# Kernel optimization log

Hardware: AMD Instinct MI355X
Metric: run time of the kernel (lower is better)

The kernel has to match this reference:

```python
import jax, jax.numpy as jnp
import numpy as np

NEG_SLOPE = 0.2  # PyG GATConv default negative_slope


def _gat_conv(x, src, dst, W, a_src, a_dst, bias, heads, concat):
    """PyG-style GATConv (eval mode, self-loops already appended to src/dst).
    x: [N, Fin], W: [Fin, heads*C], a_src/a_dst: [heads, C], bias matches output.
    """
    N = x.shape[0]
    C = W.shape[1] // heads
    xw = (x @ W).reshape(N, heads, C)                      # [N, H, C]
    alpha_s = jnp.sum(xw * a_src, axis=-1)                 # [N, H]
    alpha_d = jnp.sum(xw * a_dst, axis=-1)                 # [N, H]
    e = jax.nn.leaky_relu(alpha_s[src] + alpha_d[dst], NEG_SLOPE)  # [E, H]
    # softmax over incoming edges of each destination node (numerically stable)
    m = jax.ops.segment_max(e, dst, num_segments=N)        # [N, H]
    e = jnp.exp(e - m[dst])
    denom = jax.ops.segment_sum(e, dst, num_segments=N)    # [N, H]
    alpha = e / denom[dst]                                 # [E, H]
    out = jax.ops.segment_sum(alpha[:, :, None] * xw[src], dst, num_segments=N)  # [N, H, C]
    if concat:
        out = out.reshape(N, heads * C)
    else:
        out = out.mean(axis=1)
    return out + bias


def setup_inputs() -> dict:
    key = jax.random.key(0)
    ks = jax.random.split(key, 10)
    N, E, FIN, FOUT, H1, C1 = 100000, 1600000, 128, 16, 4, 8
    x = jax.random.normal(ks[0], (N, FIN), jnp.float32)
    edge_index = jax.random.randint(ks[1], (2, E), 0, N, dtype=jnp.int32)
    W1 = jax.random.normal(ks[2], (FIN, H1 * C1), jnp.float32) / np.sqrt(FIN)
    a1_src = jax.random.normal(ks[3], (H1, C1), jnp.float32) / np.sqrt(C1)
    a1_dst = jax.random.normal(ks[4], (H1, C1), jnp.float32) / np.sqrt(C1)
    b1 = jnp.zeros((H1 * C1,), jnp.float32)
    W2 = jax.random.normal(ks[5], (H1 * C1, FOUT), jnp.float32) / np.sqrt(H1 * C1)
    a2_src = jax.random.normal(ks[6], (1, FOUT), jnp.float32) / np.sqrt(FOUT)
    a2_dst = jax.random.normal(ks[7], (1, FOUT), jnp.float32) / np.sqrt(FOUT)
    b2 = jnp.zeros((FOUT,), jnp.float32)
    return {"x": x, "edge_index": edge_index, "W1": W1, "a1_src": a1_src,
            "a1_dst": a1_dst, "b1": b1, "W2": W2, "a2_src": a2_src,
            "a2_dst": a2_dst, "b2": b2}


def reference(x, edge_index, W1, a1_src, a1_dst, b1, W2, a2_src, a2_dst, b2):
    N = x.shape[0]
    # PyG GATConv add_self_loops=True default
    loop = jnp.arange(N, dtype=edge_index.dtype)
    src = jnp.concatenate([edge_index[0], loop])
    dst = jnp.concatenate([edge_index[1], loop])
    # eval mode: F.dropout is identity
    h = _gat_conv(x, src, dst, W1, a1_src, a1_dst, b1, heads=4, concat=True)
    h = jax.nn.elu(h)
    h = _gat_conv(h, src, dst, W2, a2_src, a2_dst, b2, heads=1, concat=True)
    return jax.nn.log_softmax(h, axis=1)
```

## Files before the change

### kernel.cpp

```cpp
#include <hip/hip_runtime.h>
#include <math.h>

#define NN 100000
#define NE 1600000
#define ET (NE + NN)
#define FIN 128
#define H1 4
#define C1 8
#define F1 32
#define FOUT 16
#define NSLOPE 0.2f

#define PARTW 256
#define PSHIFT 8
#define NPART ((NN + PARTW - 1) / PARTW)
#define CHUNK 8192
#define NBLK ((ET + CHUNK - 1) / CHUNK)
#define CPAD 16
#define SMASK 0x1FFFF

typedef _Float16 half8 __attribute__((ext_vector_type(8)));
typedef float f32x4 __attribute__((ext_vector_type(4)));


__device__ inline int wave_incl_scan(int v) {
#pragma unroll
    for (int off = 1; off < 64; off <<= 1) {
        int u = __shfl_up(v, off);
        if ((threadIdx.x & 63) >= off) v += u;
    }
    return v;
}

__device__ inline int block_excl_scan(int v, int* wsum, int nw) {
    int t = threadIdx.x, wid = t >> 6, lane = t & 63;
    int incl = wave_incl_scan(v);
    if (lane == 63) wsum[wid] = incl;
    __syncthreads();
    if (wid == 0) {
        int wv = (lane < nw) ? wsum[lane] : 0;
        wv = wave_incl_scan(wv);
        if (lane < nw) wsum[lane] = wv;
    }
    __syncthreads();
    return incl - v + (wid ? wsum[wid - 1] : 0);
}


__global__ __launch_bounds__(1024) void k_hist(const int* __restrict__ dstA, int* __restrict__ ptotal) {
    __shared__ int h[NPART];
    int t = threadIdx.x;
    for (int i = t; i < NPART; i += 1024) h[i] = 0;
    __syncthreads();
    int base = blockIdx.x * CHUNK;
#pragma unroll
    for (int k = 0; k < CHUNK / 1024; k++) {
        int e = base + k * 1024 + t;
        if (e < ET) {
            int d = (e < NE) ? dstA[e] : (e - NE);
            atomicAdd(&h[d >> PSHIFT], 1);
        }
    }
    __syncthreads();
    for (int i = t; i < NPART; i += 1024)
        if (h[i]) atomicAdd(&ptotal[i * CPAD], h[i]);
}

__global__ __launch_bounds__(512) void k_pbase(const int* __restrict__ ptotal, int* __restrict__ pbase,
                                               int* __restrict__ gcur, int* __restrict__ rowstart) {
    __shared__ int wsum[8];
    int t = threadIdx.x;
    int v = (t < NPART) ? ptotal[t * CPAD] : 0;
    int excl = block_excl_scan(v, wsum, 8);
    if (t < NPART) { pbase[t] = excl; gcur[t * CPAD] = excl; }
    if (t == 0) { pbase[NPART] = ET; rowstart[NN] = ET; }
}

__global__ __launch_bounds__(1024) void k_part(const int* __restrict__ srcA, const int* __restrict__ dstA,
                                               int* __restrict__ gcur, int* __restrict__ pairs) {
    __shared__ int h[NPART];
    __shared__ int cur[NPART];
    int t = threadIdx.x;
    for (int i = t; i < NPART; i += 1024) h[i] = 0;
    __syncthreads();
    int base = blockIdx.x * CHUNK;
#pragma unroll
    for (int k = 0; k < CHUNK / 1024; k++) {
        int e = base + k * 1024 + t;
        if (e < ET) {
            int d = (e < NE) ? dstA[e] : (e - NE);
            atomicAdd(&h[d >> PSHIFT], 1);
        }
    }
    __syncthreads();
    for (int i = t; i < NPART; i += 1024) {
        int c = h[i];
        cur[i] = c ? atomicAdd(&gcur[i * CPAD], c) : 0;
    }
    __syncthreads();
#pragma unroll
    for (int k = 0; k < CHUNK / 1024; k++) {
        int e = base + k * 1024 + t;
        if (e < ET) {
            int s, d;
            if (e < NE) { s = srcA[e]; d = dstA[e]; }
            else        { s = e - NE;  d = s; }
            int pos = atomicAdd(&cur[d >> PSHIFT], 1);
            pairs[pos] = ((d & (PARTW - 1)) << 17) | s;
        }
    }
}

__global__ __launch_bounds__(1024) void k_sort(const int* __restrict__ pbase, const int* __restrict__ pairs,
                                               int* __restrict__ rowstart, int* __restrict__ epack) {
    __shared__ int hist[PARTW];
    __shared__ int sa[PARTW], sb[PARTW];
    int p = blockIdx.x;
    int t = threadIdx.x;
    int n0 = p << PSHIFT;
    int nn = min(PARTW, NN - n0);
    int base = pbase[p];
    int cnt = pbase[p + 1] - base;
    if (t < PARTW) hist[t] = 0;
    __syncthreads();
    for (int i = t; i < cnt; i += 1024)
        atomicAdd(&hist[pairs[base + i] >> 17], 1);
    __syncthreads();
    if (t < PARTW) sa[t] = hist[t];
    __syncthreads();
    int* pin = sa; int* pout = sb;
    for (int off = 1; off < PARTW; off <<= 1) {
        if (t < PARTW) pout[t] = pin[t] + ((t >= off) ? pin[t - off] : 0);
        __syncthreads();
        int* tmp = pin; pin = pout; pout = tmp;
    }
    int excl = 0;
    if (t < PARTW) {
        excl = pin[t] - hist[t];
        if (t < nn) rowstart[n0 + t] = base + excl;
    }
    __syncthreads();
    if (t < PARTW) hist[t] = excl;
    __syncthreads();
    for (int i = t; i < cnt; i += 1024) {
        int v = pairs[base + i];
        int pos = base + atomicAdd(&hist[v >> 17], 1);
        epack[pos] = v;
    }
}


__global__ __launch_bounds__(256) void k_gemm1(const float* __restrict__ x, const float* __restrict__ W1,
        const float* __restrict__ a1s, const float* __restrict__ a1d,
        _Float16* __restrict__ xw1h, float* __restrict__ as1, float* __restrict__ ad1) {
    __shared__ _Float16 w1t[F1 * FIN];
    __shared__ float xs[256 * F1];
    int t = threadIdx.x;
    {
        int i0 = t * 16;
#pragma unroll
        for (int i = 0; i < 16; i++) {
            int idx = i0 + i;
            int k = idx >> 5, n = idx & 31;
            w1t[n * FIN + k] = (_Float16)W1[idx];
        }
    }
    __syncthreads();
    int w = t >> 6, l = t & 63;
    int q = l >> 4, r16 = l & 15;
    int nblk = blockIdx.x * 256;
    int n0 = nblk + w * 64;
    half8 bf[4][2];
#pragma unroll
    for (int kc = 0; kc < 4; kc++)
#pragma unroll
        for (int nt = 0; nt < 2; nt++)
            bf[kc][nt] = *(const half8*)&w1t[(nt * 16 + r16) * FIN + kc * 32 + q * 8];
#pragma unroll
    for (int mt = 0; mt < 4; mt++) {
        int row = n0 + mt * 16 + r16;
        int rowc = min(row, NN - 1);
        const float4* xp = (const float4*)(x + (size_t)rowc * FIN + q * 8);
        half8 af[4];
#pragma unroll
        for (int kc = 0; kc < 4; kc++) {
            float4 u = xp[kc * 8];
            float4 v = xp[kc * 8 + 1];
            half8 a;
            a[0] = (_Float16)u.x; a[1] = (_Float16)u.y; a[2] = (_Float16)u.z; a[3] = (_Float16)u.w;
            a[4] = (_Float16)v.x; a[5] = (_Float16)v.y; a[6] = (_Float16)v.z; a[7] = (_Float16)v.w;
            af[kc] = a;
        }
        f32x4 acc0 = {0.f, 0.f, 0.f, 0.f};
        f32x4 acc1 = {0.f, 0.f, 0.f, 0.f};
#pragma unroll
        for (int kc = 0; kc < 4; kc++) {
            acc0 = __builtin_amdgcn_mfma_f32_16x16x32_f16(af[kc], bf[kc][0], acc0, 0, 0, 0);
            acc1 = __builtin_amdgcn_mfma_f32_16x16x32_f16(af[kc], bf[kc][1], acc1, 0, 0, 0);
        }
#pragma unroll
        for (int r = 0; r < 4; r++) {
            xs[(w * 64 + mt * 16 + q * 4 + r) * F1 + r16] = acc0[r];
            xs[(w * 64 + mt * 16 + q * 4 + r) * F1 + 16 + r16] = acc1[r];
        }
    }
    int node = nblk + w * 64 + l;
    if (node < NN) {
        const float4* xr = (const float4*)&xs[(w * 64 + l) * F1];
        float rowv[F1];
#pragma unroll
        for (int j = 0; j < 8; j++) {
            float4 v = xr[j];
            rowv[j * 4] = v.x; rowv[j * 4 + 1] = v.y; rowv[j * 4 + 2] = v.z; rowv[j * 4 + 3] = v.w;
        }
        half8* o8 = (half8*)(xw1h + (size_t)node * F1);
#pragma unroll
        for (int c8 = 0; c8 < F1 / 8; c8++) {
            half8 o;
#pragma unroll
            for (int k = 0; k < 8; k++) o[k] = (_Float16)rowv[c8 * 8 + k];
            o8[c8] = o;
        }
        float ss[H1], dd[H1];
#pragma unroll
        for (int h = 0; h < H1; h++) {
            ss[h] = 0.f; dd[h] = 0.f;
#pragma unroll
            for (int c = 0; c < C1; c++) {
                ss[h] = fmaf(rowv[h * C1 + c], a1s[h * C1 + c], ss[h]);
                dd[h] = fmaf(rowv[h * C1 + c], a1d[h * C1 + c], dd[h]);
            }
        }
        ((float4*)as1)[node] = make_float4(ss[0], ss[1], ss[2], ss[3]);
        ((float4*)ad1)[node] = make_float4(dd[0], dd[1], dd[2], dd[3]);
    }
}


__global__ __launch_bounds__(256) void k_gather1(const int* __restrict__ rowstart, const int* __restrict__ epack,
        const float* __restrict__ as1, const float* __restrict__ ad1,
        const _Float16* __restrict__ xw1h, const float* __restrict__ b1,
        _Float16* __restrict__ h1h) {
    int n = blockIdx.x * 4 + (threadIdx.x >> 6);
    if (n >= NN) return;
    int l = threadIdx.x & 63;
    int c = l & 31;
    int h = c >> 3;
    int half = l >> 5;
    float adh = ad1[n * H1 + h];
    int beg = rowstart[n], end = rowstart[n + 1];
    float accn = 0.f, accd = 0.f;
    int i = beg + half;
    for (; i + 6 < end; i += 8) {
        int s0 = epack[i] & SMASK, s1 = epack[i + 2] & SMASK;
        int s2 = epack[i + 4] & SMASK, s3 = epack[i + 6] & SMASK;
        float e0 = as1[s0 * H1 + h] + adh;
        float e1 = as1[s1 * H1 + h] + adh;
        float e2 = as1[s2 * H1 + h] + adh;
        float e3 = as1[s3 * H1 + h] + adh;
        float x0 = (float)xw1h[s0 * F1 + c];
        float x1 = (float)xw1h[s1 * F1 + c];
        float x2 = (float)xw1h[s2 * F1 + c];
        float x3 = (float)xw1h[s3 * F1 + c];
        e0 = (e0 > 0.f) ? e0 : NSLOPE * e0;
        e1 = (e1 > 0.f) ? e1 : NSLOPE * e1;
        e2 = (e2 > 0.f) ? e2 : NSLOPE * e2;
        e3 = (e3 > 0.f) ? e3 : NSLOPE * e3;
        float ee0 = __expf(e0), ee1 = __expf(e1), ee2 = __expf(e2), ee3 = __expf(e3);
        accd += (ee0 + ee1) + (ee2 + ee3);
        accn = fmaf(ee0, x0, fmaf(ee1, x1, fmaf(ee2, x2, fmaf(ee3, x3, accn))));
    }
    for (; i < end; i += 2) {
        int s0 = epack[i] & SMASK;
        float e0 = as1[s0 * H1 + h] + adh;
        float x0 = (float)xw1h[s0 * F1 + c];
        e0 = (e0 > 0.f) ? e0 : NSLOPE * e0;
        float ee0 = __expf(e0);
        accd += ee0;
        accn = fmaf(ee0, x0, accn);
    }
    accn += __shfl_xor(accn, 32);
    accd += __shfl_xor(accd, 32);
    float y = accn / accd + b1[c];
    y = (y > 0.f) ? y : expm1f(y);
    if (l < 32) h1h[(size_t)n * F1 + c] = (_Float16)y;
}


__global__ __launch_bounds__(256) void k_node2(const _Float16* __restrict__ h1h, const float* __restrict__ W2,
        const float* __restrict__ a2s, const float* __restrict__ a2d,
        _Float16* __restrict__ xw2h, float* __restrict__ as2, float* __restrict__ ad2) {
    int n = blockIdx.x * 256 + threadIdx.x;
    if (n >= NN) return;
    float acc[FOUT];
#pragma unroll
    for (int j = 0; j < FOUT; j++) acc[j] = 0.f;
    const half8* h8 = (const half8*)(h1h + (size_t)n * F1);
#pragma unroll
    for (int i8 = 0; i8 < F1 / 8; i8++) {
        half8 hv = h8[i8];
#pragma unroll
        for (int kk = 0; kk < 8; kk++) {
            float hk = (float)hv[kk];
            int i = i8 * 8 + kk;
#pragma unroll
            for (int j = 0; j < FOUT; j++)
                acc[j] = fmaf(hk, W2[i * FOUT + j], acc[j]);
        }
    }
    float ss = 0.f, dd = 0.f;
#pragma unroll
    for (int j = 0; j < FOUT; j++) {
        ss = fmaf(acc[j], a2s[j], ss);
        dd = fmaf(acc[j], a2d[j], dd);
    }
    half8* o8 = (half8*)(xw2h + (size_t)n * FOUT);
#pragma unroll
    for (int j8 = 0; j8 < FOUT / 8; j8++) {
        half8 o;
#pragma unroll
        for (int k = 0; k < 8; k++) o[k] = (_Float16)acc[j8 * 8 + k];
        o8[j8] = o;
    }
    as2[n] = ss;
    ad2[n] = dd;
}


__global__ __launch_bounds__(256) void k_gather2(const int* __restrict__ rowstart, const int* __restrict__ epack,
        const float* __restrict__ as2, const float* __restrict__ ad2,
        const _Float16* __restrict__ xw2h, const float* __restrict__ b2,
        float* __restrict__ out) {
    int n = blockIdx.x * 4 + (threadIdx.x >> 6);
    if (n >= NN) return;
    int l = threadIdx.x & 63;
    int c = l & 15;
    int q = l >> 4;
    float adn = ad2[n];
    int beg = rowstart[n], end = rowstart[n + 1];
    float accn = 0.f, accd = 0.f;
    int i = beg + q;
    for (; i + 12 < end; i += 16) {
        int s0 = epack[i] & SMASK, s1 = epack[i + 4] & SMASK;
        int s2 = epack[i + 8] & SMASK, s3 = epack[i + 12] & SMASK;
        float e0 = as2[s0] + adn;
        float e1 = as2[s1] + adn;
        float e2 = as2[s2] + adn;
        float e3 = as2[s3] + adn;
        float x0 = (float)xw2h[s0 * FOUT + c];
        float x1 = (float)xw2h[s1 * FOUT + c];
        float x2 = (float)xw2h[s2 * FOUT + c];
        float x3 = (float)xw2h[s3 * FOUT + c];
        e0 = (e0 > 0.f) ? e0 : NSLOPE * e0;
        e1 = (e1 > 0.f) ? e1 : NSLOPE * e1;
        e2 = (e2 > 0.f) ? e2 : NSLOPE * e2;
        e3 = (e3 > 0.f) ? e3 : NSLOPE * e3;
        float ee0 = __expf(e0), ee1 = __expf(e1), ee2 = __expf(e2), ee3 = __expf(e3);
        accd += (ee0 + ee1) + (ee2 + ee3);
        accn = fmaf(ee0, x0, fmaf(ee1, x1, fmaf(ee2, x2, fmaf(ee3, x3, accn))));
    }
    for (; i < end; i += 4) {
        int s0 = epack[i] & SMASK;
        float e0 = as2[s0] + adn;
        float x0 = (float)xw2h[s0 * FOUT + c];
        e0 = (e0 > 0.f) ? e0 : NSLOPE * e0;
        float ee0 = __expf(e0);
        accd += ee0;
        accn = fmaf(ee0, x0, accn);
    }
    accn += __shfl_xor(accn, 16);
    accn += __shfl_xor(accn, 32);
    accd += __shfl_xor(accd, 16);
    accd += __shfl_xor(accd, 32);
    float y = accn / accd + b2[c];
    float m = y;
#pragma unroll
    for (int off = 8; off > 0; off >>= 1) m = fmaxf(m, __shfl_xor(m, off));
    float ex = __expf(y - m);
    float sum = ex;
#pragma unroll
    for (int off = 8; off > 0; off >>= 1) sum += __shfl_xor(sum, off);
    if (l < 16) out[(size_t)n * FOUT + c] = y - m - logf(sum);
}


extern "C" void kernel_launch(void* const* d_in, const int* in_sizes, int n_in,
                              void* d_out, int out_size, void* d_ws, size_t ws_size,
                              hipStream_t stream) {
    const float* x   = (const float*)d_in[0];
    const int*   ei  = (const int*)d_in[1];
    const float* W1  = (const float*)d_in[2];
    const float* a1s = (const float*)d_in[3];
    const float* a1d = (const float*)d_in[4];
    const float* b1  = (const float*)d_in[5];
    const float* W2  = (const float*)d_in[6];
    const float* a2s = (const float*)d_in[7];
    const float* a2d = (const float*)d_in[8];
    const float* b2  = (const float*)d_in[9];
    float* out = (float*)d_out;

    const int* srcA = ei;
    const int* dstA = ei + NE;

    char* w = (char*)d_ws;
    size_t off = 0;
    auto carve = [&](size_t bytes) -> void* {
        void* p = w + off;
        off = (off + bytes + 255) & ~(size_t)255;
        return p;
    };
    _Float16* xw1h = (_Float16*)carve((size_t)NN * F1 * 2);
    float* as1     = (float*)carve((size_t)NN * H1 * 4);
    float* ad1     = (float*)carve((size_t)NN * H1 * 4);
    size_t h1_off  = off;
    _Float16* h1h  = (_Float16*)carve((size_t)NN * F1 * 2);
    _Float16* xw2h = (_Float16*)carve((size_t)NN * FOUT * 2);
    float* as2     = (float*)carve((size_t)NN * 4);
    float* ad2     = (float*)carve((size_t)NN * 4);
    int* pairs     = (int*)(w + h1_off);
    int* rowstart  = (int*)carve((size_t)(NN + 1) * 4);
    int* epack     = (int*)carve((size_t)ET * 4);
    int* ptotal    = (int*)carve((size_t)NPART * CPAD * 4);
    int* gcur      = (int*)carve((size_t)NPART * CPAD * 4);
    int* pbase     = (int*)carve((size_t)(NPART + 1) * 4);
    (void)ws_size; (void)in_sizes; (void)n_in; (void)out_size;

    hipMemsetAsync(ptotal, 0, (size_t)NPART * CPAD * 4, stream);

    k_hist  <<<NBLK, 1024, 0, stream>>>(dstA, ptotal);
    k_pbase <<<1, 512, 0, stream>>>(ptotal, pbase, gcur, rowstart);
    k_part  <<<NBLK, 1024, 0, stream>>>(srcA, dstA, gcur, pairs);
    k_sort  <<<NPART, 1024, 0, stream>>>(pbase, pairs, rowstart, epack);

    k_gemm1 <<<(NN + 255) / 256, 256, 0, stream>>>(x, W1, a1s, a1d, xw1h, as1, ad1);
    k_gather1<<<(NN + 3) / 4, 256, 0, stream>>>(rowstart, epack, as1, ad1, xw1h, b1, h1h);
    k_node2 <<<(NN + 255) / 256, 256, 0, stream>>>(h1h, W2, a2s, a2d, xw2h, as2, ad2);
    k_gather2<<<(NN + 3) / 4, 256, 0, stream>>>(rowstart, epack, as2, ad2, xw2h, b2, out);
}
```

Baseline: 257.6 us.

## Fuse CSR build and first GEMM into one cooperative kernel with grid syncs

Replaces the memset, histogram, partition-base scan, partition scatter, per-partition sort and first-layer GEMM kernels with a single cooperative kernel of 512 blocks of 256 threads. The stages are separated by grid-wide syncs, and the partition scan now runs as a single wave. The aim is to remove several kernel launches and their inter-kernel gaps. In exchange, each stage now uses smaller blocks (the sort uses 256 threads per partition instead of 1024), every stage pays a grid-sync cost, and the whole grid must stay co-resident.

After: 501.1 us. +94.5%, slower.

```diff
diff --git a/kernel.cpp b/kernel.cpp
--- a/kernel.cpp
+++ b/kernel.cpp
@@ -1,5 +1,8 @@
 #include <hip/hip_runtime.h>
+#include <hip/hip_cooperative_groups.h>
 #include <math.h>
+
+namespace cg = cooperative_groups;
 
 #define NN 100000
 #define NE 1600000
@@ -14,14 +17,14 @@
 #define PARTW 256
 #define PSHIFT 8
 #define NPART ((NN + PARTW - 1) / PARTW)
-#define CHUNK 8192
-#define NBLK ((ET + CHUNK - 1) / CHUNK)
 #define CPAD 16
 #define SMASK 0x1FFFF
 
+#define K1B 512
+#define EB ((ET + K1B - 1) / K1B)
+
 typedef _Float16 half8 __attribute__((ext_vector_type(8)));
 typedef float f32x4 __attribute__((ext_vector_type(4)));
-
 
 __device__ inline int wave_incl_scan(int v) {
 #pragma unroll
@@ -32,207 +35,186 @@
     return v;
 }
 
-__device__ inline int block_excl_scan(int v, int* wsum, int nw) {
-    int t = threadIdx.x, wid = t >> 6, lane = t & 63;
-    int incl = wave_incl_scan(v);
-    if (lane == 63) wsum[wid] = incl;
-    __syncthreads();
-    if (wid == 0) {
-        int wv = (lane < nw) ? wsum[lane] : 0;
-        wv = wave_incl_scan(wv);
-        if (lane < nw) wsum[lane] = wv;
-    }
-    __syncthreads();
-    return incl - v + (wid ? wsum[wid - 1] : 0);
-}
-
-
-__global__ __launch_bounds__(1024) void k_hist(const int* __restrict__ dstA, int* __restrict__ ptotal) {
-    __shared__ int h[NPART];
-    int t = threadIdx.x;
-    for (int i = t; i < NPART; i += 1024) h[i] = 0;
-    __syncthreads();
-    int base = blockIdx.x * CHUNK;
-#pragma unroll
-    for (int k = 0; k < CHUNK / 1024; k++) {
-        int e = base + k * 1024 + t;
-        if (e < ET) {
-            int d = (e < NE) ? dstA[e] : (e - NE);
-            atomicAdd(&h[d >> PSHIFT], 1);
-        }
-    }
-    __syncthreads();
-    for (int i = t; i < NPART; i += 1024)
-        if (h[i]) atomicAdd(&ptotal[i * CPAD], h[i]);
-}
-
-__global__ __launch_bounds__(512) void k_pbase(const int* __restrict__ ptotal, int* __restrict__ pbase,
-                                               int* __restrict__ gcur, int* __restrict__ rowstart) {
-    __shared__ int wsum[8];
-    int t = threadIdx.x;
-    int v = (t < NPART) ? ptotal[t * CPAD] : 0;
-    int excl = block_excl_scan(v, wsum, 8);
-    if (t < NPART) { pbase[t] = excl; gcur[t * CPAD] = excl; }
-    if (t == 0) { pbase[NPART] = ET; rowstart[NN] = ET; }
-}
-
-__global__ __launch_bounds__(1024) void k_part(const int* __restrict__ srcA, const int* __restrict__ dstA,
-                                               int* __restrict__ gcur, int* __restrict__ pairs) {
+
+__global__ __launch_bounds__(256) void k_build(const int* __restrict__ srcA, const int* __restrict__ dstA,
+        const float* __restrict__ x, const float* __restrict__ W1,
+        const float* __restrict__ a1s, const float* __restrict__ a1d,
+        int* __restrict__ ptotal, int* __restrict__ gcur, int* __restrict__ pbase,
+        int* __restrict__ rowstart, int* __restrict__ pairs, int* __restrict__ epack,
+        _Float16* __restrict__ xw1h, float* __restrict__ as1, float* __restrict__ ad1) {
+    cg::grid_group grid = cg::this_grid();
     __shared__ int h[NPART];
     __shared__ int cur[NPART];
-    int t = threadIdx.x;
-    for (int i = t; i < NPART; i += 1024) h[i] = 0;
-    __syncthreads();
-    int base = blockIdx.x * CHUNK;
-#pragma unroll
-    for (int k = 0; k < CHUNK / 1024; k++) {
-        int e = base + k * 1024 + t;
-        if (e < ET) {
-            int d = (e < NE) ? dstA[e] : (e - NE);
-            atomicAdd(&h[d >> PSHIFT], 1);
-        }
-    }
-    __syncthreads();
-    for (int i = t; i < NPART; i += 1024) {
-        int c = h[i];
-        cur[i] = c ? atomicAdd(&gcur[i * CPAD], c) : 0;
-    }
-    __syncthreads();
-#pragma unroll
-    for (int k = 0; k < CHUNK / 1024; k++) {
-        int e = base + k * 1024 + t;
-        if (e < ET) {
-            int s, d;
-            if (e < NE) { s = srcA[e]; d = dstA[e]; }
-            else        { s = e - NE;  d = s; }
-            int pos = atomicAdd(&cur[d >> PSHIFT], 1);
-            pairs[pos] = ((d & (PARTW - 1)) << 17) | s;
-        }
-    }
-}
-
-__global__ __launch_bounds__(1024) void k_sort(const int* __restrict__ pbase, const int* __restrict__ pairs,
-                                               int* __restrict__ rowstart, int* __restrict__ epack) {
-    __shared__ int hist[PARTW];
-    __shared__ int sa[PARTW], sb[PARTW];
-    int p = blockIdx.x;
-    int t = threadIdx.x;
-    int n0 = p << PSHIFT;
-    int nn = min(PARTW, NN - n0);
-    int base = pbase[p];
-    int cnt = pbase[p + 1] - base;
-    if (t < PARTW) hist[t] = 0;
-    __syncthreads();
-    for (int i = t; i < cnt; i += 1024)
-        atomicAdd(&hist[pairs[base + i] >> 17], 1);
-    __syncthreads();
-    if (t < PARTW) sa[t] = hist[t];
-    __syncthreads();
-    int* pin = sa; int* pout = sb;
-    for (int off = 1; off < PARTW; off <<= 1) {
-        if (t < PARTW) pout[t] = pin[t] + ((t >= off) ? pin[t - off] : 0);
-        __syncthreads();
-        int* tmp = pin; pin = pout; pout = tmp;
-    }
-    int excl = 0;
-    if (t < PARTW) {
-        excl = pin[t] - hist[t];
-        if (t < nn) rowstart[n0 + t] = base + excl;
-    }
-    __syncthreads();
-    if (t < PARTW) hist[t] = excl;
-    __syncthreads();
-    for (int i = t; i < cnt; i += 1024) {
-        int v = pairs[base + i];
-        int pos = base + atomicAdd(&hist[v >> 17], 1);
-        epack[pos] = v;
-    }
-}
-
-
-__global__ __launch_bounds__(256) void k_gemm1(const float* __restrict__ x, const float* __restrict__ W1,
-        const float* __restrict__ a1s, const float* __restrict__ a1d,
-        _Float16* __restrict__ xw1h, float* __restrict__ as1, float* __restrict__ ad1) {
+    __shared__ int sc[PARTW];
     __shared__ _Float16 w1t[F1 * FIN];
     __shared__ float xs[256 * F1];
     int t = threadIdx.x;
+    int b = blockIdx.x;
+    int e0 = b * EB, e1 = min(e0 + EB, ET);
+
     {
-        int i0 = t * 16;
-#pragma unroll
-        for (int i = 0; i < 16; i++) {
-            int idx = i0 + i;
-            int k = idx >> 5, n = idx & 31;
-            w1t[n * FIN + k] = (_Float16)W1[idx];
-        }
-    }
+        int idx = b * 256 + t;
+        if (idx < NPART) ptotal[idx * CPAD] = 0;
+    }
+    grid.sync();
+
+    for (int i = t; i < NPART; i += 256) h[i] = 0;
     __syncthreads();
-    int w = t >> 6, l = t & 63;
-    int q = l >> 4, r16 = l & 15;
-    int nblk = blockIdx.x * 256;
-    int n0 = nblk + w * 64;
-    half8 bf[4][2];
-#pragma unroll
-    for (int kc = 0; kc < 4; kc++)
-#pragma unroll
-        for (int nt = 0; nt < 2; nt++)
-            bf[kc][nt] = *(const half8*)&w1t[(nt * 16 + r16) * FIN + kc * 32 + q * 8];
-#pragma unroll
-    for (int mt = 0; mt < 4; mt++) {
-        int row = n0 + mt * 16 + r16;
-        int rowc = min(row, NN - 1);
-        const float4* xp = (const float4*)(x + (size_t)rowc * FIN + q * 8);
-        half8 af[4];
-#pragma unroll
-        for (int kc = 0; kc < 4; kc++) {
-            float4 u = xp[kc * 8];
-            float4 v = xp[kc * 8 + 1];
-            half8 a;
-            a[0] = (_Float16)u.x; a[1] = (_Float16)u.y; a[2] = (_Float16)u.z; a[3] = (_Float16)u.w;
-            a[4] = (_Float16)v.x; a[5] = (_Float16)v.y; a[6] = (_Float16)v.z; a[7] = (_Float16)v.w;
-            af[kc] = a;
-        }
-        f32x4 acc0 = {0.f, 0.f, 0.f, 0.f};
-        f32x4 acc1 = {0.f, 0.f, 0.f, 0.f};
-#pragma unroll
-        for (int kc = 0; kc < 4; kc++) {
-            acc0 = __builtin_amdgcn_mfma_f32_16x16x32_f16(af[kc], bf[kc][0], acc0, 0, 0, 0);
-            acc1 = __builtin_amdgcn_mfma_f32_16x16x32_f16(af[kc], bf[kc][1], acc1, 0, 0, 0);
-        }
-#pragma unroll
-        for (int r = 0; r < 4; r++) {
-            xs[(w * 64 + mt * 16 + q * 4 + r) * F1 + r16] = acc0[r];
-            xs[(w * 64 + mt * 16 + q * 4 + r) * F1 + 16 + r16] = acc1[r];
-        }
-    }
-    int node = nblk + w * 64 + l;
-    if (node < NN) {
-        const float4* xr = (const float4*)&xs[(w * 64 + l) * F1];
-        float rowv[F1];
-#pragma unroll
-        for (int j = 0; j < 8; j++) {
-            float4 v = xr[j];
-            rowv[j * 4] = v.x; rowv[j * 4 + 1] = v.y; rowv[j * 4 + 2] = v.z; rowv[j * 4 + 3] = v.w;
-        }
-        half8* o8 = (half8*)(xw1h + (size_t)node * F1);
-#pragma unroll
-        for (int c8 = 0; c8 < F1 / 8; c8++) {
-            half8 o;
-#pragma unroll
-            for (int k = 0; k < 8; k++) o[k] = (_Float16)rowv[c8 * 8 + k];
-            o8[c8] = o;
-        }
-        float ss[H1], dd[H1];
-#pragma unroll
-        for (int h = 0; h < H1; h++) {
-            ss[h] = 0.f; dd[h] = 0.f;
-#pragma unroll
-            for (int c = 0; c < C1; c++) {
-                ss[h] = fmaf(rowv[h * C1 + c], a1s[h * C1 + c], ss[h]);
-                dd[h] = fmaf(rowv[h * C1 + c], a1d[h * C1 + c], dd[h]);
-            }
-        }
-        ((float4*)as1)[node] = make_float4(ss[0], ss[1], ss[2], ss[3]);
-        ((float4*)ad1)[node] = make_float4(dd[0], dd[1], dd[2], dd[3]);
+    for (int e = e0 + t; e < e1; e += 256) {
+        int d = (e < NE) ? dstA[e] : (e - NE);
+        atomicAdd(&h[d >> PSHIFT], 1);
+    }
+    __syncthreads();
+    for (int i = t; i < NPART; i += 256)
+        if (h[i]) atomicAdd(&ptotal[i * CPAD], h[i]);
+    grid.sync();
+
+    if (b == 0 && t < 64) {
+        int base = t * 7;
+        int loc[7]; int s = 0;
+#pragma unroll
+        for (int i = 0; i < 7; i++) {
+            int idx = base + i;
+            int v = (idx < NPART) ? ptotal[idx * CPAD] : 0;
+            loc[i] = s; s += v;
+        }
+        int wex = wave_incl_scan(s) - s;
+#pragma unroll
+        for (int i = 0; i < 7; i++) {
+            int idx = base + i;
+            if (idx < NPART) { pbase[idx] = wex + loc[i]; gcur[idx * CPAD] = wex + loc[i]; }
+        }
+        if (t == 0) { pbase[NPART] = ET; rowstart[NN] = ET; }
+    }
+    grid.sync();
+
+    for (int i = t; i < NPART; i += 256) {
+        int c = h[i];
+        cur[i] = c ? atomicAdd(&gcur[i * CPAD], c) : 0;
+    }
+    __syncthreads();
+    for (int e = e0 + t; e < e1; e += 256) {
+        int s, d;
+        if (e < NE) { s = srcA[e]; d = dstA[e]; }
+        else        { s = e - NE;  d = s; }
+        int pos = atomicAdd(&cur[d >> PSHIFT], 1);
+        pairs[pos] = ((d & (PARTW - 1)) << 17) | s;
+    }
+    grid.sync();
+
+    if (b < NPART) {
+        int n0 = b << PSHIFT;
+        int nn = min(PARTW, NN - n0);
+        int base = pbase[b];
+        int cnt = pbase[b + 1] - base;
+        if (t < PARTW) h[t] = 0;
+        __syncthreads();
+        for (int i = t; i < cnt; i += 256)
+            atomicAdd(&h[pairs[base + i] >> 17], 1);
+        __syncthreads();
+        if (t < PARTW) cur[t] = h[t];
+        __syncthreads();
+        int* pin = cur; int* pout = sc;
+        for (int off = 1; off < PARTW; off <<= 1) {
+            if (t < PARTW) pout[t] = pin[t] + ((t >= off) ? pin[t - off] : 0);
+            __syncthreads();
+            int* tmp = pin; pin = pout; pout = tmp;
+        }
+        int excl = 0;
+        if (t < PARTW) {
+            excl = pin[t] - h[t];
+            if (t < nn) rowstart[n0 + t] = base + excl;
+        }
+        __syncthreads();
+        if (t < PARTW) h[t] = excl;
+        __syncthreads();
+        for (int i = t; i < cnt; i += 256) {
+            int v = pairs[base + i];
+            int pos = base + atomicAdd(&h[v >> 17], 1);
+            epack[pos] = v;
+        }
+        __syncthreads();
+    }
+
+    if (b * 256 < NN) {
+        {
+            int i0 = t * 16;
+#pragma unroll
+            for (int i = 0; i < 16; i++) {
+                int idx = i0 + i;
+                int k = idx >> 5, n = idx & 31;
+                w1t[n * FIN + k] = (_Float16)W1[idx];
+            }
+        }
+        __syncthreads();
+        int w = t >> 6, l = t & 63;
+        int q = l >> 4, r16 = l & 15;
+        int nblk = b * 256;
+        int n0 = nblk + w * 64;
+        half8 bf[4][2];
+#pragma unroll
+        for (int kc = 0; kc < 4; kc++)
+#pragma unroll
+            for (int nt = 0; nt < 2; nt++)
+                bf[kc][nt] = *(const half8*)&w1t[(nt * 16 + r16) * FIN + kc * 32 + q * 8];
+#pragma unroll
+        for (int mt = 0; mt < 4; mt++) {
+            int row = n0 + mt * 16 + r16;
+            int rowc = min(row, NN - 1);
+            const float4* xp = (const float4*)(x + (size_t)rowc * FIN + q * 8);
+            half8 af[4];
+#pragma unroll
+            for (int kc = 0; kc < 4; kc++) {
+                float4 u = xp[kc * 8];
+                float4 v = xp[kc * 8 + 1];
+                half8 a;
+                a[0] = (_Float16)u.x; a[1] = (_Float16)u.y; a[2] = (_Float16)u.z; a[3] = (_Float16)u.w;
+                a[4] = (_Float16)v.x; a[5] = (_Float16)v.y; a[6] = (_Float16)v.z; a[7] = (_Float16)v.w;
+                af[kc] = a;
+            }
+            f32x4 acc0 = {0.f, 0.f, 0.f, 0.f};
+            f32x4 acc1 = {0.f, 0.f, 0.f, 0.f};
+#pragma unroll
+            for (int kc = 0; kc < 4; kc++) {
+                acc0 = __builtin_amdgcn_mfma_f32_16x16x32_f16(af[kc], bf[kc][0], acc0, 0, 0, 0);
+                acc1 = __builtin_amdgcn_mfma_f32_16x16x32_f16(af[kc], bf[kc][1], acc1, 0, 0, 0);
+            }
+#pragma unroll
+            for (int r = 0; r < 4; r++) {
+                xs[(w * 64 + mt * 16 + q * 4 + r) * F1 + r16] = acc0[r];
+                xs[(w * 64 + mt * 16 + q * 4 + r) * F1 + 16 + r16] = acc1[r];
+            }
+        }
+        int node = nblk + w * 64 + l;
+        if (node < NN) {
+            const float4* xr = (const float4*)&xs[(w * 64 + l) * F1];
+            float rowv[F1];
+#pragma unroll
+            for (int j = 0; j < 8; j++) {
+                float4 v = xr[j];
+                rowv[j * 4] = v.x; rowv[j * 4 + 1] = v.y; rowv[j * 4 + 2] = v.z; rowv[j * 4 + 3] = v.w;
+            }
+            half8* o8 = (half8*)(xw1h + (size_t)node * F1);
+#pragma unroll
+            for (int c8 = 0; c8 < F1 / 8; c8++) {
+                half8 o;
+#pragma unroll
+                for (int k = 0; k < 8; k++) o[k] = (_Float16)rowv[c8 * 8 + k];
+                o8[c8] = o;
+            }
+            float ss[H1], dd[H1];
+#pragma unroll
+            for (int hh = 0; hh < H1; hh++) {
+                ss[hh] = 0.f; dd[hh] = 0.f;
+#pragma unroll
+                for (int c = 0; c < C1; c++) {
+                    ss[hh] = fmaf(rowv[hh * C1 + c], a1s[hh * C1 + c], ss[hh]);
+                    dd[hh] = fmaf(rowv[hh * C1 + c], a1d[hh * C1 + c], dd[hh]);
+                }
+            }
+            ((float4*)as1)[node] = make_float4(ss[0], ss[1], ss[2], ss[3]);
+            ((float4*)ad1)[node] = make_float4(dd[0], dd[1], dd[2], dd[3]);
+        }
     }
 }
 
@@ -425,14 +407,12 @@
     int* pbase     = (int*)carve((size_t)(NPART + 1) * 4);
     (void)ws_size; (void)in_sizes; (void)n_in; (void)out_size;
 
-    hipMemsetAsync(ptotal, 0, (size_t)NPART * CPAD * 4, stream);
-
-    k_hist  <<<NBLK, 1024, 0, stream>>>(dstA, ptotal);
-    k_pbase <<<1, 512, 0, stream>>>(ptotal, pbase, gcur, rowstart);
-    k_part  <<<NBLK, 1024, 0, stream>>>(srcA, dstA, gcur, pairs);
-    k_sort  <<<NPART, 1024, 0, stream>>>(pbase, pairs, rowstart, epack);
-
-    k_gemm1 <<<(NN + 255) / 256, 256, 0, stream>>>(x, W1, a1s, a1d, xw1h, as1, ad1);
+    void* args[] = { (void*)&srcA, (void*)&dstA, (void*)&x, (void*)&W1,
+                     (void*)&a1s, (void*)&a1d, (void*)&ptotal, (void*)&gcur,
+                     (void*)&pbase, (void*)&rowstart, (void*)&pairs, (void*)&epack,
+                     (void*)&xw1h, (void*)&as1, (void*)&ad1 };
+    hipLaunchCooperativeKernel((const void*)k_build, dim3(K1B), dim3(256), args, 0, stream);
+
     k_gather1<<<(NN + 3) / 4, 256, 0, stream>>>(rowstart, epack, as1, ad1, xw1h, b1, h1h);
     k_node2 <<<(NN + 255) / 256, 256, 0, stream>>>(h1h, W2, a2s, a2d, xw2h, as2, ad2);
     k_gather2<<<(NN + 3) / 4, 256, 0, stream>>>(rowstart, epack, as2, ad2, xw2h, b2, out);
```
